# Optimization experiments

Hardware: AMD Instinct MI355X
Metric: run time of the kernel (lower is better)

Reference implementation:

```python
import jax, jax.numpy as jnp
import numpy as np

ALPHA = 1.0
BETA = 1.0
B, C, F = 16384, 2000, 1024

def setup_inputs() -> dict:
    key = jax.random.key(0)
    k1, k2, k3, k4 = jax.random.split(key, 4)
    features = jax.random.normal(k1, (B, F), dtype=jnp.float32)
    labels = jax.random.randint(k2, (B,), 0, C, dtype=jnp.int64)
    centers = jax.random.normal(k3, (C, F), dtype=jnp.float32)
    W = jax.random.normal(k4, (C, F), dtype=jnp.float32) * (1.0 / np.sqrt(F))
    b = jnp.zeros((C,), dtype=jnp.float32)
    return {"features": features, "labels": labels, "centers": centers, "W": W, "b": b}

def reference(features, labels, centers, W, b):
    # Fisher (center) loss: only the true-class center distance is used, so
    # gather centers[labels] instead of materializing the [B, C, F] broadcast.
    diff = features - centers[labels]                     # [B, F]
    fisher_loss = jnp.mean(jnp.sum(diff * diff, axis=1))  # scalar
    # Aux cross-entropy over a linear classifier.
    logits = jnp.einsum('bf,cf->bc', features, W) + b     # [B, C]
    logZ = jax.nn.logsumexp(logits, axis=1)               # [B]
    true_logit = jnp.take_along_axis(logits, labels[:, None], axis=1)[:, 0]
    aux_loss = jnp.mean(logZ - true_logit)
    return ALPHA * fisher_loss + BETA * aux_loss
```

## Files before the change

### kernel.cpp

```cpp
#include <hip/hip_runtime.h>
#include <stdint.h>

#define B_ROWS 16384
#define C_CLS  2000
#define C_PAD  2048
#define F_DIM  1024
#define KT     16
#define NRB    64
#define NCBP   16
#define PANEL_A 262144
#define PANEL_BB 131072

typedef float f32x16 __attribute__((ext_vector_type(16)));
typedef int   i32x4  __attribute__((ext_vector_type(4)));
typedef int   i32x8  __attribute__((ext_vector_type(8)));

#define SCALE_F 4.0f
#define SCALE_W 16.0f
#define INV_SCALE 0.015625f
#define SCL1 0x7F7F7F7F

__device__ __forceinline__ unsigned int pk4(float a, float b, float c, float d) {
    int u = __builtin_amdgcn_cvt_pk_fp8_f32(a, b, 0, false);
    u = __builtin_amdgcn_cvt_pk_fp8_f32(c, d, u, true);
    return (unsigned int)u;
}


__global__ __launch_bounds__(256)
void prep_kernel(const float* __restrict__ feat, const int* __restrict__ labels,
                 const float* __restrict__ centers, const float* __restrict__ W,
                 const float* __restrict__ bias,
                 char* __restrict__ A_pre, char* __restrict__ B_pre,
                 float* __restrict__ bias_pad, float* __restrict__ fisher_part)
{
    const int tid = threadIdx.x;
    if (blockIdx.x < 512) {
        const int rt = blockIdx.x >> 2, g = blockIdx.x & 3;
        const int rb = rt >> 1;
        const int r = tid >> 1, h = tid & 1;
        const int grow = rt * 128 + r;
        const int lab = labels[grow];
        const float* frow = feat    + (size_t)grow * F_DIM;
        const float* crow = centers + (size_t)lab  * F_DIM;
        const int f = (rt & 1) * 4 + (r >> 5);
        const int lane = (h << 5) | (r & 31);
        char* pbase = A_pre + (size_t)rb * PANEL_A + f * 2048 + lane * 32;
        float facc = 0.f;
        #pragma unroll
        for (int q = 0; q < 4; ++q) {
            const int kt = g * 4 + q;
            const int k0 = kt * 64 + h * 32;
            unsigned int o[8];
            #pragma unroll
            for (int c = 0; c < 8; ++c) {
                float4 av = *(const float4*)(frow + k0 + c * 4);
                float4 cv = *(const float4*)(crow + k0 + c * 4);
                float d0 = av.x - cv.x, d1 = av.y - cv.y, d2 = av.z - cv.z, d3 = av.w - cv.w;
                facc += d0 * d0 + d1 * d1 + d2 * d2 + d3 * d3;
                o[c] = pk4(SCALE_F * av.x, SCALE_F * av.y, SCALE_F * av.z, SCALE_F * av.w);
            }
            char* dst = pbase + kt * 16384;
            *(uint4*)(dst)      = (uint4){o[0], o[1], o[2], o[3]};
            *(uint4*)(dst + 16) = (uint4){o[4], o[5], o[6], o[7]};
        }
        for (int d = 32; d >= 1; d >>= 1) facc += __shfl_xor(facc, d);
        __shared__ float redw[4];
        const int wid = tid >> 6, ln = tid & 63;
        if (ln == 0) redw[wid] = facc;
        __syncthreads();
        if (tid == 0) fisher_part[blockIdx.x] = redw[0] + redw[1] + redw[2] + redw[3];
    } else {
        const int b = blockIdx.x - 512;
        const int ct = b >> 3, ktg = b & 7;
        const int cb = ct >> 1;
        const int rcol = tid >> 1, h = tid & 1;
        const int gc = ct * 128 + rcol;
        const int f = (ct & 1) * 2 + (rcol >> 5);
        const int lane = (h << 5) | (rcol & 31);
        char* pbase = B_pre + (size_t)cb * PANEL_BB + f * 2048 + lane * 32;
        #pragma unroll
        for (int q = 0; q < 2; ++q) {
            const int kt = ktg * 2 + q;
            const int k0 = kt * 64 + h * 32;
            unsigned int o[8];
            if (gc < C_CLS) {
                const float* src = W + (size_t)gc * F_DIM + k0;
                #pragma unroll
                for (int c = 0; c < 8; ++c) {
                    float4 av = *(const float4*)(src + c * 4);
                    o[c] = pk4(SCALE_W * av.x, SCALE_W * av.y, SCALE_W * av.z, SCALE_W * av.w);
                }
            } else {
                #pragma unroll
                for (int c = 0; c < 8; ++c) o[c] = 0u;
            }
            char* dst = pbase + kt * 8192;
            *(uint4*)(dst)      = (uint4){o[0], o[1], o[2], o[3]};
            *(uint4*)(dst + 16) = (uint4){o[4], o[5], o[6], o[7]};
        }
        if (b < C_PAD / 256) {
            const int i = b * 256 + tid;
            bias_pad[i] = (i < C_CLS) ? bias[i] : -1e30f;
        }
    }
}

__global__ __launch_bounds__(256, 2)
void gemm_kernel(const int* __restrict__ labels, const float* __restrict__ biasp,
                 const char* __restrict__ A_pre, const char* __restrict__ B_pre,
                 float* __restrict__ s_part, float* __restrict__ tl_part)
{
    const int cpx = gridDim.x >> 3;
    const int wg = (blockIdx.x & 7) * cpx + (blockIdx.x >> 3);
    const int cb = wg & 15;
    const int rb = wg >> 4;

    const int tid = threadIdx.x;
    const int w = tid >> 6, lane = tid & 63;
    const int l31 = lane & 31, lh = lane >> 5;

    const char* Apan = A_pre + (size_t)rb * PANEL_A + w * 4096 + lane * 32;
    const char* Bpan = B_pre + (size_t)cb * PANEL_BB + lane * 32;

    f32x16 acc[2][4];
    #pragma unroll
    for (int mi = 0; mi < 2; ++mi)
        #pragma unroll
        for (int ni = 0; ni < 4; ++ni)
            #pragma unroll
            for (int e = 0; e < 16; ++e) acc[mi][ni][e] = 0.f;

    i32x8 aE[2], bE[4], aO[2], bO[4];

#define LOAD32B(DST, P) do {                                                          \
    *(i32x4*)&(DST)       = *(const i32x4*)(P);                                       \
    *(((i32x4*)&(DST))+1) = *(const i32x4*)((P) + 16);                                \
} while (0)

#define LOADT(SA, SB, KTT) do {                                                       \
    const char* pa_ = Apan + (KTT) * 16384;                                           \
    const char* pb_ = Bpan + (KTT) * 8192;                                            \
    _Pragma("unroll")                                                                 \
    for (int i_ = 0; i_ < 2; ++i_) LOAD32B(SA[i_], pa_ + i_ * 2048);                  \
    _Pragma("unroll")                                                                 \
    for (int i_ = 0; i_ < 4; ++i_) LOAD32B(SB[i_], pb_ + i_ * 2048);                  \
} while (0)

#define MFMA8(SA, SB) do {                                                            \
    __builtin_amdgcn_s_setprio(1);                                                    \
    _Pragma("unroll")                                                                 \
    for (int mi_ = 0; mi_ < 2; ++mi_)                                                 \
        _Pragma("unroll")                                                             \
        for (int ni_ = 0; ni_ < 4; ++ni_)                                             \
            acc[mi_][ni_] = __builtin_amdgcn_mfma_scale_f32_32x32x64_f8f6f4(          \
                SA[mi_], SB[ni_], acc[mi_][ni_], 0, 0, 0, SCL1, 0, SCL1);             \
    __builtin_amdgcn_s_setprio(0);                                                    \
} while (0)

#define FENCE __builtin_amdgcn_sched_barrier(0)

    LOADT(aE, bE, 0);
    FENCE;
    #pragma unroll 1
    for (int k2 = 0; k2 < 7; ++k2) {
        LOADT(aO, bO, 2 * k2 + 1);
        FENCE;
        MFMA8(aE, bE);
        FENCE;
        LOADT(aE, bE, 2 * k2 + 2);
        FENCE;
        MFMA8(aO, bO);
        FENCE;
    }
    LOADT(aO, bO, 15);
    FENCE;
    MFMA8(aE, bE);
    MFMA8(aO, bO);

#undef LOADT
#undef LOAD32B
#undef MFMA8
#undef FENCE

    float bb[4];
    #pragma unroll
    for (int ni = 0; ni < 4; ++ni)
        bb[ni] = biasp[cb * 128 + ni * 32 + l31];

    #pragma unroll
    for (int mi = 0; mi < 2; ++mi) {
        #pragma unroll
        for (int reg = 0; reg < 16; ++reg) {
            const int rl = w * 64 + mi * 32 + (reg & 3) + 8 * (reg >> 2) + 4 * lh;
            const int lab = labels[rb * 256 + rl];
            float sv = 0.f, tv = 0.f;
            #pragma unroll
            for (int ni = 0; ni < 4; ++ni) {
                const float v = fmaf(acc[mi][ni][reg], INV_SCALE, bb[ni]);
                sv += __expf(v);
                const int gc = cb * 128 + ni * 32 + l31;
                tv = (gc == lab) ? v : tv;
            }
            #pragma unroll
            for (int d = 1; d < 32; d <<= 1) {
                sv += __shfl_xor(sv, d);
                tv += __shfl_xor(tv, d);
            }
            if (l31 == 0) {
                const int grow = rb * 256 + rl;
                s_part[(size_t)cb * B_ROWS + grow]  = sv;
                tl_part[(size_t)cb * B_ROWS + grow] = tv;
            }
        }
    }
}

__global__ __launch_bounds__(256)
void rowcomb_kernel(const float* __restrict__ s_part, const float* __restrict__ tl_part,
                    float* __restrict__ aux_part)
{
    const int row = blockIdx.x * 256 + threadIdx.x;
    float s = 0.f, t = 0.f;
    #pragma unroll
    for (int p = 0; p < NCBP; ++p) {
        s += s_part[(size_t)p * B_ROWS + row];
        t += tl_part[(size_t)p * B_ROWS + row];
    }
    float acc = __logf(s) - t;
    for (int d = 32; d >= 1; d >>= 1) acc += __shfl_xor(acc, d);
    __shared__ float red[4];
    const int wid = threadIdx.x >> 6, lane = threadIdx.x & 63;
    if (lane == 0) red[wid] = acc;
    __syncthreads();
    if (threadIdx.x == 0) aux_part[blockIdx.x] = red[0] + red[1] + red[2] + red[3];
}

__global__ __launch_bounds__(256)
void final_kernel(const float* __restrict__ fisher_part, const float* __restrict__ aux_part,
                  float* __restrict__ out)
{
    const int tid = threadIdx.x;
    float acc = fisher_part[tid] + fisher_part[256 + tid];
    if (tid < 64) acc += aux_part[tid];
    for (int d = 32; d >= 1; d >>= 1) acc += __shfl_xor(acc, d);
    __shared__ float red[4];
    const int wid = tid >> 6, lane = tid & 63;
    if (lane == 0) red[wid] = acc;
    __syncthreads();
    if (tid == 0) out[0] = (red[0] + red[1] + red[2] + red[3]) * (1.0f / (float)B_ROWS);
}

extern "C" void kernel_launch(void* const* d_in, const int* in_sizes, int n_in,
                              void* d_out, int out_size, void* d_ws, size_t ws_size,
                              hipStream_t stream)
{
    (void)in_sizes; (void)n_in; (void)out_size; (void)ws_size;
    const float* feat    = (const float*)d_in[0];
    const int*   labels  = (const int*)  d_in[1];
    const float* centers = (const float*)d_in[2];
    const float* W       = (const float*)d_in[3];
    const float* bias    = (const float*)d_in[4];
    float* out = (float*)d_out;
    char* ws = (char*)d_ws;

    const size_t szA    = (size_t)NRB  * PANEL_A;
    const size_t szB    = (size_t)NCBP * PANEL_BB;
    const size_t szBias = (size_t)C_PAD * 4;

    char* A_pre = ws;
    char* B_pre = ws + szA;
    float* bias_pad    = (float*)(ws + szA + szB);
    float* s_part      = (float*)(ws + szA + szB + szBias);
    float* tl_part     = s_part + (size_t)NCBP * B_ROWS;
    float* fisher_part = tl_part + (size_t)NCBP * B_ROWS;
    float* aux_part    = fisher_part + 512;

    prep_kernel<<<640, 256, 0, stream>>>(feat, labels, centers, W, bias,
                                         A_pre, B_pre, bias_pad, fisher_part);
    gemm_kernel<<<NRB * NCBP, 256, 0, stream>>>(labels, bias_pad, A_pre, B_pre, s_part, tl_part);
    rowcomb_kernel<<<B_ROWS / 256, 256, 0, stream>>>(s_part, tl_part, aux_part);
    final_kernel<<<1, 256, 0, stream>>>(fisher_part, aux_part, out);
}
```

Before: 95.18 us.

## Stage FP8 GEMM tiles through LDS with direct global-to-LDS loads and 128x128 tiles

The GEMM now uses 128x128 workgroup tiles instead of 256x128, with each wave computing a 64x64 sub-tile. Previously each wave loaded its MFMA fragments straight from global memory into registers. Now A and B k-tiles are double-buffered in LDS using global_load_lds, and the prep kernel writes an XOR-swizzled layout to avoid LDS bank conflicts. The aim is to share B across waves and raise occupancy. In exchange it adds a barrier every k-step, doubles the partial softmax sums that rowcomb must reduce, and does less MFMA work per load.

```diff
diff --git a/kernel.cpp b/kernel.cpp
--- a/kernel.cpp
+++ b/kernel.cpp
@@ -6,10 +6,11 @@
 #define C_PAD  2048
 #define F_DIM  1024
 #define KT     16
-#define NRB    64
-#define NCBP   16
-#define PANEL_A 262144
-#define PANEL_BB 131072
+#define NRB    128
+#define NCB    16
+#define NPART  32
+#define IMG_B  8192
+#define PANEL  ((size_t)KT * IMG_B)
 
 typedef float f32x16 __attribute__((ext_vector_type(16)));
 typedef int   i32x4  __attribute__((ext_vector_type(4)));
@@ -20,12 +21,19 @@
 #define INV_SCALE 0.015625f
 #define SCL1 0x7F7F7F7F
 
+__device__ __forceinline__ void gl_lds16(const void* g, void* l) {
+    __builtin_amdgcn_global_load_lds(
+        (const __attribute__((address_space(1))) unsigned int*)g,
+        (__attribute__((address_space(3))) unsigned int*)l, 16, 0, 0);
+}
+
 __device__ __forceinline__ unsigned int pk4(float a, float b, float c, float d) {
     int u = __builtin_amdgcn_cvt_pk_fp8_f32(a, b, 0, false);
     u = __builtin_amdgcn_cvt_pk_fp8_f32(c, d, u, true);
     return (unsigned int)u;
 }
 
+__device__ __forceinline__ int chpos(int c) { return c ^ ((c >> 3) & 7); }
 
 __global__ __launch_bounds__(256)
 void prep_kernel(const float* __restrict__ feat, const int* __restrict__ labels,
@@ -37,15 +45,14 @@
     const int tid = threadIdx.x;
     if (blockIdx.x < 512) {
         const int rt = blockIdx.x >> 2, g = blockIdx.x & 3;
-        const int rb = rt >> 1;
         const int r = tid >> 1, h = tid & 1;
         const int grow = rt * 128 + r;
         const int lab = labels[grow];
         const float* frow = feat    + (size_t)grow * F_DIM;
         const float* crow = centers + (size_t)lab  * F_DIM;
-        const int f = (rt & 1) * 4 + (r >> 5);
-        const int lane = (h << 5) | (r & 31);
-        char* pbase = A_pre + (size_t)rb * PANEL_A + f * 2048 + lane * 32;
+        const int frag = r >> 5;
+        const int c0 = 2 * (h * 32 + (r & 31));
+        char* fbase = A_pre + (size_t)rt * PANEL + frag * 2048;
         float facc = 0.f;
         #pragma unroll
         for (int q = 0; q < 4; ++q) {
@@ -60,9 +67,9 @@
                 facc += d0 * d0 + d1 * d1 + d2 * d2 + d3 * d3;
                 o[c] = pk4(SCALE_F * av.x, SCALE_F * av.y, SCALE_F * av.z, SCALE_F * av.w);
             }
-            char* dst = pbase + kt * 16384;
-            *(uint4*)(dst)      = (uint4){o[0], o[1], o[2], o[3]};
-            *(uint4*)(dst + 16) = (uint4){o[4], o[5], o[6], o[7]};
+            char* dst = fbase + (size_t)kt * IMG_B;
+            *(uint4*)(dst + chpos(c0) * 16)     = (uint4){o[0], o[1], o[2], o[3]};
+            *(uint4*)(dst + chpos(c0 + 1) * 16) = (uint4){o[4], o[5], o[6], o[7]};
         }
         for (int d = 32; d >= 1; d >>= 1) facc += __shfl_xor(facc, d);
         __shared__ float redw[4];
@@ -73,12 +80,11 @@
     } else {
         const int b = blockIdx.x - 512;
         const int ct = b >> 3, ktg = b & 7;
-        const int cb = ct >> 1;
         const int rcol = tid >> 1, h = tid & 1;
         const int gc = ct * 128 + rcol;
-        const int f = (ct & 1) * 2 + (rcol >> 5);
-        const int lane = (h << 5) | (rcol & 31);
-        char* pbase = B_pre + (size_t)cb * PANEL_BB + f * 2048 + lane * 32;
+        const int frag = rcol >> 5;
+        const int c0 = 2 * (h * 32 + (rcol & 31));
+        char* fbase = B_pre + (size_t)ct * PANEL + frag * 2048;
         #pragma unroll
         for (int q = 0; q < 2; ++q) {
             const int kt = ktg * 2 + q;
@@ -95,9 +101,9 @@
                 #pragma unroll
                 for (int c = 0; c < 8; ++c) o[c] = 0u;
             }
-            char* dst = pbase + kt * 8192;
-            *(uint4*)(dst)      = (uint4){o[0], o[1], o[2], o[3]};
-            *(uint4*)(dst + 16) = (uint4){o[4], o[5], o[6], o[7]};
+            char* dst = fbase + (size_t)kt * IMG_B;
+            *(uint4*)(dst + chpos(c0) * 16)     = (uint4){o[0], o[1], o[2], o[3]};
+            *(uint4*)(dst + chpos(c0 + 1) * 16) = (uint4){o[4], o[5], o[6], o[7]};
         }
         if (b < C_PAD / 256) {
             const int i = b * 256 + tid;
@@ -111,6 +117,8 @@
                  const char* __restrict__ A_pre, const char* __restrict__ B_pre,
                  float* __restrict__ s_part, float* __restrict__ tl_part)
 {
+    __shared__ alignas(128) char smem[2][16384];
+
     const int cpx = gridDim.x >> 3;
     const int wg = (blockIdx.x & 7) * cpx + (blockIdx.x >> 3);
     const int cb = wg & 15;
@@ -119,87 +127,81 @@
     const int tid = threadIdx.x;
     const int w = tid >> 6, lane = tid & 63;
     const int l31 = lane & 31, lh = lane >> 5;
-
-    const char* Apan = A_pre + (size_t)rb * PANEL_A + w * 4096 + lane * 32;
-    const char* Bpan = B_pre + (size_t)cb * PANEL_BB + lane * 32;
-
-    f32x16 acc[2][4];
+    const int wr = w >> 1, wc = w & 1;
+
+    const char* Asrc = A_pre + (size_t)rb * PANEL;
+    const char* Bsrc = B_pre + (size_t)cb * PANEL;
+
+    const int off0 = chpos(2 * lane) * 16;
+
+    f32x16 acc[2][2];
     #pragma unroll
     for (int mi = 0; mi < 2; ++mi)
         #pragma unroll
-        for (int ni = 0; ni < 4; ++ni)
+        for (int ni = 0; ni < 2; ++ni)
             #pragma unroll
             for (int e = 0; e < 16; ++e) acc[mi][ni][e] = 0.f;
 
-    i32x8 aE[2], bE[4], aO[2], bO[4];
-
-#define LOAD32B(DST, P) do {                                                          \
-    *(i32x4*)&(DST)       = *(const i32x4*)(P);                                       \
-    *(((i32x4*)&(DST))+1) = *(const i32x4*)((P) + 16);                                \
+#define STAGE(KTT, BUF) do {                                                          \
+    const char* sa_ = Asrc + (size_t)(KTT) * IMG_B + tid * 16;                        \
+    const char* sb_ = Bsrc + (size_t)(KTT) * IMG_B + tid * 16;                        \
+    char* da_ = smem[BUF] + w * 1024;                                                 \
+    gl_lds16(sa_,        da_);                                                        \
+    gl_lds16(sa_ + 4096, da_ + 4096);                                                 \
+    gl_lds16(sb_,        da_ + 8192);                                                 \
+    gl_lds16(sb_ + 4096, da_ + 12288);                                                \
 } while (0)
 
-#define LOADT(SA, SB, KTT) do {                                                       \
-    const char* pa_ = Apan + (KTT) * 16384;                                           \
-    const char* pb_ = Bpan + (KTT) * 8192;                                            \
-    _Pragma("unroll")                                                                 \
-    for (int i_ = 0; i_ < 2; ++i_) LOAD32B(SA[i_], pa_ + i_ * 2048);                  \
-    _Pragma("unroll")                                                                 \
-    for (int i_ = 0; i_ < 4; ++i_) LOAD32B(SB[i_], pb_ + i_ * 2048);                  \
+#define RDFRAG(DST, BASE) do {                                                        \
+    *(i32x4*)&(DST)       = *(const i32x4*)((BASE) + off0);                           \
+    *(((i32x4*)&(DST))+1) = *(const i32x4*)((BASE) + (off0 ^ 16));                    \
 } while (0)
 
-#define MFMA8(SA, SB) do {                                                            \
-    __builtin_amdgcn_s_setprio(1);                                                    \
-    _Pragma("unroll")                                                                 \
-    for (int mi_ = 0; mi_ < 2; ++mi_)                                                 \
-        _Pragma("unroll")                                                             \
-        for (int ni_ = 0; ni_ < 4; ++ni_)                                             \
-            acc[mi_][ni_] = __builtin_amdgcn_mfma_scale_f32_32x32x64_f8f6f4(          \
-                SA[mi_], SB[ni_], acc[mi_][ni_], 0, 0, 0, SCL1, 0, SCL1);             \
-    __builtin_amdgcn_s_setprio(0);                                                    \
-} while (0)
-
-#define FENCE __builtin_amdgcn_sched_barrier(0)
-
-    LOADT(aE, bE, 0);
-    FENCE;
+    STAGE(0, 0);
+    __syncthreads();
+
     #pragma unroll 1
-    for (int k2 = 0; k2 < 7; ++k2) {
-        LOADT(aO, bO, 2 * k2 + 1);
-        FENCE;
-        MFMA8(aE, bE);
-        FENCE;
-        LOADT(aE, bE, 2 * k2 + 2);
-        FENCE;
-        MFMA8(aO, bO);
-        FENCE;
-    }
-    LOADT(aO, bO, 15);
-    FENCE;
-    MFMA8(aE, bE);
-    MFMA8(aO, bO);
-
-#undef LOADT
-#undef LOAD32B
-#undef MFMA8
-#undef FENCE
-
-    float bb[4];
-    #pragma unroll
-    for (int ni = 0; ni < 4; ++ni)
-        bb[ni] = biasp[cb * 128 + ni * 32 + l31];
-
+    for (int kt = 0; kt < KT; ++kt) {
+        const int cur = kt & 1;
+        if (kt + 1 < KT) STAGE(kt + 1, cur ^ 1);
+        const char* Ab = smem[cur] + wr * 4096;
+        const char* Bb = smem[cur] + 8192 + wc * 4096;
+        i32x8 af[2], bf[2];
+        RDFRAG(af[0], Ab);
+        RDFRAG(af[1], Ab + 2048);
+        RDFRAG(bf[0], Bb);
+        RDFRAG(bf[1], Bb + 2048);
+        __builtin_amdgcn_s_setprio(1);
+        #pragma unroll
+        for (int mi = 0; mi < 2; ++mi)
+            #pragma unroll
+            for (int ni = 0; ni < 2; ++ni)
+                acc[mi][ni] = __builtin_amdgcn_mfma_scale_f32_32x32x64_f8f6f4(
+                    af[mi], bf[ni], acc[mi][ni], 0, 0, 0, SCL1, 0, SCL1);
+        __builtin_amdgcn_s_setprio(0);
+        __syncthreads();
+    }
+#undef STAGE
+#undef RDFRAG
+
+    float bb[2];
+    #pragma unroll
+    for (int ni = 0; ni < 2; ++ni)
+        bb[ni] = biasp[cb * 128 + wc * 64 + ni * 32 + l31];
+
+    const int pidx = cb * 2 + wc;
     #pragma unroll
     for (int mi = 0; mi < 2; ++mi) {
         #pragma unroll
         for (int reg = 0; reg < 16; ++reg) {
-            const int rl = w * 64 + mi * 32 + (reg & 3) + 8 * (reg >> 2) + 4 * lh;
-            const int lab = labels[rb * 256 + rl];
+            const int rl = wr * 64 + mi * 32 + (reg & 3) + 8 * (reg >> 2) + 4 * lh;
+            const int lab = labels[rb * 128 + rl];
             float sv = 0.f, tv = 0.f;
             #pragma unroll
-            for (int ni = 0; ni < 4; ++ni) {
+            for (int ni = 0; ni < 2; ++ni) {
                 const float v = fmaf(acc[mi][ni][reg], INV_SCALE, bb[ni]);
                 sv += __expf(v);
-                const int gc = cb * 128 + ni * 32 + l31;
+                const int gc = cb * 128 + wc * 64 + ni * 32 + l31;
                 tv = (gc == lab) ? v : tv;
             }
             #pragma unroll
@@ -208,9 +210,9 @@
                 tv += __shfl_xor(tv, d);
             }
             if (l31 == 0) {
-                const int grow = rb * 256 + rl;
-                s_part[(size_t)cb * B_ROWS + grow]  = sv;
-                tl_part[(size_t)cb * B_ROWS + grow] = tv;
+                const int grow = rb * 128 + rl;
+                s_part[(size_t)pidx * B_ROWS + grow]  = sv;
+                tl_part[(size_t)pidx * B_ROWS + grow] = tv;
             }
         }
     }
@@ -223,7 +225,7 @@
     const int row = blockIdx.x * 256 + threadIdx.x;
     float s = 0.f, t = 0.f;
     #pragma unroll
-    for (int p = 0; p < NCBP; ++p) {
+    for (int p = 0; p < NPART; ++p) {
         s += s_part[(size_t)p * B_ROWS + row];
         t += tl_part[(size_t)p * B_ROWS + row];
     }
@@ -264,21 +266,22 @@
     float* out = (float*)d_out;
     char* ws = (char*)d_ws;
 
-    const size_t szA    = (size_t)NRB  * PANEL_A;
-    const size_t szB    = (size_t)NCBP * PANEL_BB;
+    const size_t szA    = (size_t)NRB * PANEL;
+    const size_t szB    = (size_t)NCB * PANEL;
     const size_t szBias = (size_t)C_PAD * 4;
+    const size_t szPart = (size_t)NPART * B_ROWS * 4;
 
     char* A_pre = ws;
     char* B_pre = ws + szA;
     float* bias_pad    = (float*)(ws + szA + szB);
     float* s_part      = (float*)(ws + szA + szB + szBias);
-    float* tl_part     = s_part + (size_t)NCBP * B_ROWS;
-    float* fisher_part = tl_part + (size_t)NCBP * B_ROWS;
+    float* tl_part     = (float*)(ws + szA + szB + szBias + szPart);
+    float* fisher_part = (float*)(ws + szA + szB + szBias + 2 * szPart);
     float* aux_part    = fisher_part + 512;
 
     prep_kernel<<<640, 256, 0, stream>>>(feat, labels, centers, W, bias,
                                          A_pre, B_pre, bias_pad, fisher_part);
-    gemm_kernel<<<NRB * NCBP, 256, 0, stream>>>(labels, bias_pad, A_pre, B_pre, s_part, tl_part);
+    gemm_kernel<<<NRB * NCB, 256, 0, stream>>>(labels, bias_pad, A_pre, B_pre, s_part, tl_part);
     rowcomb_kernel<<<B_ROWS / 256, 256, 0, stream>>>(s_part, tl_part, aux_part);
     final_kernel<<<1, 256, 0, stream>>>(fisher_part, aux_part, out);
 }
```

Measured after the change: 118.4 us. +24.4%, slower.
